# Kernel optimization log

Hardware: AMD Instinct MI355X
Metric: run time of the kernel (lower is better)

The kernel has to match this reference:

```python
import jax, jax.numpy as jnp
import numpy as np

B, L, D, K = 4, 512, 768, 96
H = 4 * D  # projection hidden width


def _proj(x, w1, b1, w2, b2):
    # create_projection_layer: Linear -> ReLU -> (Dropout, identity at eval) -> Linear
    return jnp.maximum(x @ w1 + b1, 0.0) @ w2 + b2


def setup_inputs() -> dict:
    key = jax.random.key(0)
    ks = jax.random.split(key, 12)
    g = lambda k, shape, fan: jax.random.normal(k, shape, jnp.float32) * (1.0 / np.sqrt(fan))
    inp = {
        "h": jax.random.normal(ks[0], (B, L, D), jnp.float32),
        "span_idx": jax.random.randint(ks[1], (B, K, 2), 0, L),
        "ps_w1": g(ks[2], (D, H), D), "ps_b1": jnp.zeros((H,), jnp.float32),
        "ps_w2": g(ks[3], (H, D), H), "ps_b2": jnp.zeros((D,), jnp.float32),
        "pe_w1": g(ks[4], (D, H), D), "pe_b1": jnp.zeros((H,), jnp.float32),
        "pe_w2": g(ks[5], (H, D), H), "pe_b2": jnp.zeros((D,), jnp.float32),
        "so_w1": g(ks[6], (2 * D, H), 2 * D), "so_b1": jnp.zeros((H,), jnp.float32),
        "so_w2": g(ks[7], (H, D), H), "so_b2": jnp.zeros((D,), jnp.float32),
        "ro_w1": g(ks[8], (2 * D, H), 2 * D), "ro_b1": jnp.zeros((H,), jnp.float32),
        "ro_w2": g(ks[9], (H, D), H), "ro_b2": jnp.zeros((D,), jnp.float32),
    }
    return inp


def _gather_tokens(rep, idx):
    # rep: [B,L,D], idx: [B,K] -> [B,K,D]
    b, k = idx.shape
    d = rep.shape[-1]
    return jnp.take_along_axis(rep, jnp.broadcast_to(idx[:, :, None], (b, k, d)), axis=1)


def reference(h, span_idx, ps_w1, ps_b1, ps_w2, ps_b2, pe_w1, pe_b1, pe_w2, pe_b2,
              so_w1, so_b1, so_w2, so_b2, ro_w1, ro_b1, ro_w2, ro_b2):
    # SpanMarkerV1
    start_rep = _proj(h, ps_w1, ps_b1, ps_w2, ps_b2)   # [B,L,D]
    end_rep = _proj(h, pe_w1, pe_b1, pe_w2, pe_b2)     # [B,L,D]
    st = _gather_tokens(start_rep, span_idx[:, :, 0])  # [B,K,D]
    en = _gather_tokens(end_rep, span_idx[:, :, 1])    # [B,K,D]
    cat = jnp.maximum(jnp.concatenate([st, en], axis=-1), 0.0)  # relu
    entity_reps = _proj(cat, so_w1, so_b1, so_w2, so_b2)        # [B,K,D]

    # off-diagonal pair enumeration, row-major (i,j) with i != j — static indices
    n = entity_reps.shape[1]
    idx = np.arange(n)
    ii = np.repeat(idx, n)
    jj = np.tile(idx, n)
    keep = ii != jj
    ii, jj = ii[keep], jj[keep]  # each length n*(n-1)
    pairs = jnp.concatenate([entity_reps[:, ii], entity_reps[:, jj]], axis=-1)  # [B,P,2D]
    return _proj(pairs, ro_w1, ro_b1, ro_w2, ro_b2)  # [B,P,D]
```

## Files before the change

### kernel.cpp

```cpp
#include <hip/hip_runtime.h>
#include <hip/hip_bf16.h>

#define Bdim 4
#define Ldim 512
#define Ddim 768
#define Kspan 96
#define Hdim 3072
#define Pdim 9120
#define MROWS 384
#define NKT 96

typedef __bf16 bf16x8 __attribute__((ext_vector_type(8)));
typedef float f32x4 __attribute__((ext_vector_type(4)));
typedef float f32x16 __attribute__((ext_vector_type(16)));
typedef unsigned short ushort8v __attribute__((ext_vector_type(8)));
typedef unsigned short ushort4v __attribute__((ext_vector_type(4)));

static __device__ __forceinline__ unsigned short f2bf(float x){
  return __builtin_bit_cast(unsigned short, (__bf16)x);
}
static __device__ __forceinline__ float bf2f(unsigned short u){
  return (float)__builtin_bit_cast(__bf16, u);
}

__global__ __launch_bounds__(256) void transpose_split(
    const float* __restrict__ W, unsigned short* __restrict__ WTh,
    unsigned short* __restrict__ WTl, int K, int N)
{
  __shared__ float tile[64][65];
  int k0 = blockIdx.y * 64, n0 = blockIdx.x * 64;
  int c = threadIdx.x & 63, r0 = threadIdx.x >> 6;
  for (int p = 0; p < 16; p++){
    int r = r0 + p * 4;
    tile[c][r] = W[(size_t)(k0 + r) * N + n0 + c];
  }
  __syncthreads();
  for (int p = 0; p < 16; p++){
    int n = r0 + p * 4;
    float x = tile[n][c];
    unsigned short h = f2bf(x);
    size_t o = (size_t)(n0 + n) * K + k0 + c;
    WTh[o] = h;
    WTl[o] = f2bf(x - bf2f(h));
  }
}

__global__ __launch_bounds__(256) void pack_w2(
    const float* __restrict__ W, unsigned short* __restrict__ W2P)
{
  __shared__ float tile[32][97];
  int kt = blockIdx.x, nq = blockIdx.y, t = threadIdx.x;
  for (int q = 0; q < 12; q++){
    int flat = q * 256 + t;
    int kl = flat / 96, n = flat - kl * 96;
    tile[kl][n] = W[(size_t)(kt * 32 + kl) * Ddim + nq * 96 + n];
  }
  __syncthreads();
  unsigned short* outp = W2P + ((size_t)(nq * 96 + kt)) * 3072;
  for (int q = 0; q < 12; q++){
    int o = q * 256 + t;
    int n = o >> 5, klx = o & 31;
    int kl = klx ^ ((n & 8) << 1);
    outp[o] = f2bf(tile[kl][n]);
  }
}

__global__ __launch_bounds__(256) void pack_v(
    const float* __restrict__ Vbuf, unsigned short* __restrict__ Vp)
{
  int kt = blockIdx.x, b = blockIdx.y, t = threadIdx.x;
  unsigned short* outp = Vp + ((size_t)(b * 96 + kt)) * 3072;
  for (int q = 0; q < 12; q++){
    int flat = q * 256 + t;
    int j = flat >> 5, kl = flat & 31;
    outp[flat] = f2bf(Vbuf[(size_t)(b * 96 + j) * Hdim + kt * 32 + kl]);
  }
}

__global__ __launch_bounds__(256) void gather_rows(
    const float* __restrict__ h, const int* __restrict__ span, float* __restrict__ hg)
{
  int x = blockIdx.x;
  int sel = (x >= MROWS) ? 1 : 0;
  int r = x - sel * MROWS;
  int b = r / Kspan, k = r - b * Kspan;
  int idx = span[(b * Kspan + k) * 2 + sel];
  const float* src = h + ((size_t)b * Ldim + idx) * Ddim;
  float* dst = hg + (size_t)x * Ddim;
  for (int d = threadIdx.x; d < Ddim; d += 256) dst[d] = src[d];
}

struct GJob {
  const float* A;
  const unsigned short* Wh;
  const unsigned short* Wl;
  const float* bias;
  float* C;
};

template<int MODE, int SPLIT>
__global__ __launch_bounds__(256) void gemm_ms(
    GJob j0, GJob j1, int ldA, int ldW, int ldC, int kLen, size_t csz)
{
  constexpr int SR = 40;
  __shared__ __align__(16) unsigned short Ah[64 * SR], Al[64 * SR];
  __shared__ __align__(16) unsigned short Bh[128 * SR], Bl[128 * SR];
  int zj, s;
  if (SPLIT == 1){ zj = blockIdx.z; s = 0; }
  else { zj = blockIdx.z / SPLIT; s = blockIdx.z % SPLIT; }
  const GJob J = zj ? j1 : j0;
  int kBegin = s * kLen;
  float* Cptr = (MODE == 2) ? (J.C + (size_t)s * csz) : J.C;

  int m0 = blockIdx.y * 64, n0 = blockIdx.x * 128;
  int t = threadIdx.x, lane = t & 63, wid = t >> 6;
  int wm = wid >> 1, wn = wid & 1;
  int lr = lane & 15, lk = (lane >> 4) * 8;
  f32x4 acc[2][4] = {};
  int ar = t >> 2, akq = t & 3;
  for (int k0 = 0; k0 < kLen; k0 += 32){
    {
      const float* sp = J.A + (size_t)(m0 + ar) * ldA + kBegin + k0 + akq * 8;
      f32x4 x0 = *(const f32x4*)sp, x1 = *(const f32x4*)(sp + 4);
      ushort8v vh, vl;
      for (int e = 0; e < 4; e++){ float x = x0[e]; unsigned short hh = f2bf(x); vh[e] = hh; vl[e] = f2bf(x - bf2f(hh)); }
      for (int e = 0; e < 4; e++){ float x = x1[e]; unsigned short hh = f2bf(x); vh[e+4] = hh; vl[e+4] = f2bf(x - bf2f(hh)); }
      *(ushort8v*)&Ah[ar * SR + akq * 8] = vh;
      *(ushort8v*)&Al[ar * SR + akq * 8] = vl;
    }
    for (int p = 0; p < 2; p++){
      int idx = p * 256 + t; int n = idx >> 2, kq = idx & 3;
      size_t go = (size_t)(n0 + n) * ldW + kBegin + k0 + kq * 8;
      *(ushort8v*)&Bh[n * SR + kq * 8] = *(const ushort8v*)(J.Wh + go);
      *(ushort8v*)&Bl[n * SR + kq * 8] = *(const ushort8v*)(J.Wl + go);
    }
    __syncthreads();
    bf16x8 ah[2], al2[2], bh[4], bl[4];
    for (int f = 0; f < 2; f++){ int o = (wm * 32 + f * 16 + lr) * SR + lk; ah[f] = *(const bf16x8*)&Ah[o]; al2[f] = *(const bf16x8*)&Al[o]; }
    for (int g = 0; g < 4; g++){ int o = (wn * 64 + g * 16 + lr) * SR + lk; bh[g] = *(const bf16x8*)&Bh[o]; bl[g] = *(const bf16x8*)&Bl[o]; }
    for (int f = 0; f < 2; f++)
      for (int g = 0; g < 4; g++){
        acc[f][g] = __builtin_amdgcn_mfma_f32_16x16x32_bf16(ah[f],  bh[g], acc[f][g], 0, 0, 0);
        acc[f][g] = __builtin_amdgcn_mfma_f32_16x16x32_bf16(ah[f],  bl[g], acc[f][g], 0, 0, 0);
        acc[f][g] = __builtin_amdgcn_mfma_f32_16x16x32_bf16(al2[f], bh[g], acc[f][g], 0, 0, 0);
      }
    __syncthreads();
  }
  int rr = (lane >> 4) * 4;
  for (int f = 0; f < 2; f++){
    int gm = m0 + wm * 32 + f * 16 + rr;
    for (int g = 0; g < 4; g++){
      int gn = n0 + wn * 64 + g * 16 + (lane & 15);
      float bv = (MODE != 2 && J.bias) ? J.bias[gn] : 0.f;
      for (int r2 = 0; r2 < 4; r2++){
        float v = acc[f][g][r2] + bv;
        if (MODE == 0) v = fmaxf(v, 0.f);
        Cptr[(size_t)(gm + r2) * ldC + gn] = v;
      }
    }
  }
}

template<bool RELU>
__global__ __launch_bounds__(256) void reduce_part(
    const float* __restrict__ P, int S,
    const float* __restrict__ bias0, const float* __restrict__ bias1,
    float* __restrict__ outp, int zCount, int ldOut)
{
  const int MN = MROWS * Ddim;
  int idx4 = blockIdx.x * 256 + threadIdx.x;
  int flat = idx4 * 4;
  if (flat >= MN * zCount) return;
  int z = flat / MN; int rem = flat - z * MN;
  int r = rem / Ddim; int c = rem - r * Ddim;
  const float* base = P + (size_t)z * S * MN + rem;
  f32x4 sv = *(const f32x4*)base;
  for (int ss = 1; ss < S; ss++){ f32x4 v = *(const f32x4*)(base + (size_t)ss * MN); sv += v; }
  const float* bp = z ? bias1 : bias0;
  f32x4 bv = *(const f32x4*)(bp + c);
  sv += bv;
  if (RELU) for (int e = 0; e < 4; e++) sv[e] = fmaxf(sv[e], 0.f);
  *(f32x4*)(outp + (size_t)r * ldOut + z * Ddim + c) = sv;
}

__global__ __launch_bounds__(256, 2) void pair_gemm3(
    const float* __restrict__ U,
    const unsigned short* __restrict__ Vp,
    const unsigned short* __restrict__ W2P,
    const float* __restrict__ b2,
    float* __restrict__ out)
{
  __shared__ __align__(16) unsigned short As[2][384 * 32];
  __shared__ __align__(16) unsigned short Bs[2][96 * 32];

  int x = blockIdx.x;
  int nq = x & 7;
  int l = x >> 3;
  int b = l / 24;
  int iq = l - b * 24;

  int t = threadIdx.x, lane = t & 63, w = t >> 6;
  int kq = t & 7, jb = t >> 3;

  ushort4v vld[3];
  f32x4 uld[4];
  f32x16 acc[3][3] = {};

  auto issueB = [&](int kt, int buf){
    const unsigned short* tb = W2P + ((size_t)(nq * 96 + kt)) * 3072;
    #pragma unroll
    for (int s2 = 0; s2 < 2; s2++){
      int seg = w + s2 * 4;
      if (seg < 6){
        const unsigned short* src = tb + seg * 512 + lane * 8;
        unsigned int* dst = (unsigned int*)&Bs[buf][seg * 512 + lane * 8];
        __builtin_amdgcn_global_load_lds(
            (const __attribute__((address_space(1))) unsigned int*)src,
            (__attribute__((address_space(3))) unsigned int*)dst, 16, 0, 0);
      }
    }
  };
  auto issueUV = [&](int kt){
    const unsigned short* vb = Vp + ((size_t)(b * 96 + kt)) * 3072 + kq * 4;
    #pragma unroll
    for (int q = 0; q < 3; q++)
      vld[q] = *(const ushort4v*)(vb + (q * 32 + jb) * 32);
    const float* ub = U + ((size_t)(b * 96 + iq * 4)) * Hdim + kt * 32 + kq * 4;
    #pragma unroll
    for (int g = 0; g < 4; g++)
      uld[g] = *(const f32x4*)(ub + (size_t)g * Hdim);
  };
  auto buildA = [&](int buf){
    #pragma unroll
    for (int q = 0; q < 3; q++){
      int j = q * 32 + jb;
      f32x4 vf;
      #pragma unroll
      for (int e = 0; e < 4; e++) vf[e] = bf2f(vld[q][e]);
      #pragma unroll
      for (int g = 0; g < 4; g++){
        int row = g * 96 + j;
        ushort4v pk;
        #pragma unroll
        for (int e = 0; e < 4; e++) pk[e] = f2bf(fmaxf(uld[g][e] + vf[e], 0.f));
        int idx = row * 32 + ((kq * 4) ^ ((row & 8) << 1));
        *(ushort4v*)&As[buf][idx] = pk;
      }
    }
  };
  auto mfmaPhase = [&](int buf){
    #pragma unroll
    for (int kh = 0; kh < 2; kh++){
      int gg = kh * 2 + (lane >> 5);
      bf16x8 af[3], bfr[3];
      #pragma unroll
      for (int mf = 0; mf < 3; mf++){
        int row = w * 96 + mf * 32 + (lane & 31);
        af[mf] = *(const bf16x8*)&As[buf][row * 32 + ((gg * 8) ^ ((row & 8) << 1))];
      }
      #pragma unroll
      for (int nf = 0; nf < 3; nf++){
        int n = nf * 32 + (lane & 31);
        bfr[nf] = *(const bf16x8*)&Bs[buf][n * 32 + ((gg * 8) ^ ((n & 8) << 1))];
      }
      __builtin_amdgcn_s_setprio(1);
      #pragma unroll
      for (int mf = 0; mf < 3; mf++)
        #pragma unroll
        for (int nf = 0; nf < 3; nf++)
          acc[mf][nf] = __builtin_amdgcn_mfma_f32_32x32x16_bf16(af[mf], bfr[nf], acc[mf][nf], 0, 0, 0);
      __builtin_amdgcn_s_setprio(0);
    }
  };

  issueB(0, 0);
  issueUV(0);
  buildA(0);
  __syncthreads();

  for (int kt = 0; kt < NKT; kt++){
    int cur = kt & 1;
    if (kt + 1 < NKT){ issueB(kt + 1, cur ^ 1); issueUV(kt + 1); }
    mfmaPhase(cur);
    if (kt + 1 < NKT) buildA(cur ^ 1);
    __syncthreads();
  }

  int i = iq * 4 + w;
  size_t outB = (size_t)b * Pdim;
  int colbase = nq * 96;
  float bc[3];
  #pragma unroll
  for (int nf = 0; nf < 3; nf++) bc[nf] = b2[colbase + nf * 32 + (lane & 31)];
  #pragma unroll
  for (int mf = 0; mf < 3; mf++){
    #pragma unroll
    for (int reg = 0; reg < 16; reg++){
      int j = mf * 32 + (reg & 3) + 8 * (reg >> 2) + 4 * (lane >> 5);
      if (j == i) continue;
      int p = i * 95 + j - (j > i ? 1 : 0);
      float* orow = out + (outB + p) * Ddim + colbase;
      #pragma unroll
      for (int nf = 0; nf < 3; nf++){
        int cn = nf * 32 + (lane & 31);
        orow[cn] = acc[mf][nf][reg] + bc[nf];
      }
    }
  }
}

extern "C" void kernel_launch(void* const* d_in, const int* in_sizes, int n_in,
                              void* d_out, int out_size, void* d_ws, size_t ws_size,
                              hipStream_t stream)
{
  (void)in_sizes; (void)n_in; (void)out_size;
  const float* h     = (const float*)d_in[0];
  const int*   span  = (const int*)d_in[1];
  const float* ps_w1 = (const float*)d_in[2];
  const float* ps_b1 = (const float*)d_in[3];
  const float* ps_w2 = (const float*)d_in[4];
  const float* ps_b2 = (const float*)d_in[5];
  const float* pe_w1 = (const float*)d_in[6];
  const float* pe_b1 = (const float*)d_in[7];
  const float* pe_w2 = (const float*)d_in[8];
  const float* pe_b2 = (const float*)d_in[9];
  const float* so_w1 = (const float*)d_in[10];
  const float* so_b1 = (const float*)d_in[11];
  const float* so_w2 = (const float*)d_in[12];
  const float* so_b2 = (const float*)d_in[13];
  const float* ro_w1 = (const float*)d_in[14];
  const float* ro_b1 = (const float*)d_in[15];
  const float* ro_w2 = (const float*)d_in[16];
  const float* ro_b2 = (const float*)d_in[17];

  char* ws = (char*)d_ws;
  size_t off = 0;
  auto alloc_us = [&](size_t n)->unsigned short*{
    unsigned short* p = (unsigned short*)(ws + off);
    off += ((n * 2 + 255) & ~(size_t)255);
    return p;
  };
  auto alloc_f = [&](size_t n)->float*{
    float* p = (float*)(ws + off);
    off += ((n * 4 + 255) & ~(size_t)255);
    return p;
  };

  unsigned short* ps1h = alloc_us((size_t)Hdim * Ddim); unsigned short* ps1l = alloc_us((size_t)Hdim * Ddim);
  unsigned short* ps2h = alloc_us((size_t)Ddim * Hdim); unsigned short* ps2l = alloc_us((size_t)Ddim * Hdim);
  unsigned short* pe1h = alloc_us((size_t)Hdim * Ddim); unsigned short* pe1l = alloc_us((size_t)Hdim * Ddim);
  unsigned short* pe2h = alloc_us((size_t)Ddim * Hdim); unsigned short* pe2l = alloc_us((size_t)Ddim * Hdim);
  unsigned short* so1h = alloc_us((size_t)Hdim * 2 * Ddim); unsigned short* so1l = alloc_us((size_t)Hdim * 2 * Ddim);
  unsigned short* so2h = alloc_us((size_t)Ddim * Hdim); unsigned short* so2l = alloc_us((size_t)Ddim * Hdim);
  unsigned short* ro1h = alloc_us((size_t)Hdim * 2 * Ddim); unsigned short* ro1l = alloc_us((size_t)Hdim * 2 * Ddim);
  unsigned short* W2P  = alloc_us((size_t)Ddim * Hdim);
  unsigned short* Vp   = alloc_us((size_t)Bdim * Kspan * Hdim);
  float* hg     = alloc_f((size_t)2 * MROWS * Ddim);
  float* mid_s  = alloc_f((size_t)MROWS * Hdim);
  float* mid_e  = alloc_f((size_t)MROWS * Hdim);
  float* cat    = alloc_f((size_t)MROWS * 2 * Ddim);
  float* entity = alloc_f((size_t)MROWS * Ddim);
  float* Ubuf   = alloc_f((size_t)MROWS * Hdim);
  float* Vbuf   = alloc_f((size_t)MROWS * Hdim);
  const size_t MN = (size_t)MROWS * Ddim;
  float* P2 = alloc_f(8 * MN);
  float* P3 = alloc_f(4 * MN);
  if (off > ws_size) return;

  dim3 tb(256);
  transpose_split<<<dim3(Hdim/64, Ddim/64), tb, 0, stream>>>(ps_w1, ps1h, ps1l, Ddim, Hdim);
  transpose_split<<<dim3(Ddim/64, Hdim/64), tb, 0, stream>>>(ps_w2, ps2h, ps2l, Hdim, Ddim);
  transpose_split<<<dim3(Hdim/64, Ddim/64), tb, 0, stream>>>(pe_w1, pe1h, pe1l, Ddim, Hdim);
  transpose_split<<<dim3(Ddim/64, Hdim/64), tb, 0, stream>>>(pe_w2, pe2h, pe2l, Hdim, Ddim);
  transpose_split<<<dim3(Hdim/64, (2*Ddim)/64), tb, 0, stream>>>(so_w1, so1h, so1l, 2*Ddim, Hdim);
  transpose_split<<<dim3(Ddim/64, Hdim/64), tb, 0, stream>>>(so_w2, so2h, so2l, Hdim, Ddim);
  transpose_split<<<dim3(Hdim/64, (2*Ddim)/64), tb, 0, stream>>>(ro_w1, ro1h, ro1l, 2*Ddim, Hdim);
  pack_w2<<<dim3(NKT, 8), tb, 0, stream>>>(ro_w2, W2P);

  gather_rows<<<2 * MROWS, tb, 0, stream>>>(h, span, hg);

  {
    GJob j0{hg,                      ps1h, ps1l, ps_b1, mid_s};
    GJob j1{hg + (size_t)MROWS*Ddim, pe1h, pe1l, pe_b1, mid_e};
    gemm_ms<0,1><<<dim3(Hdim/128, MROWS/64, 2), tb, 0, stream>>>(j0, j1, Ddim, Ddim, Hdim, Ddim, 0);
  }
  {
    GJob j0{mid_s, ps2h, ps2l, nullptr, P2};
    GJob j1{mid_e, pe2h, pe2l, nullptr, P2 + 4*MN};
    gemm_ms<2,4><<<dim3(Ddim/128, MROWS/64, 8), tb, 0, stream>>>(j0, j1, Hdim, Hdim, Ddim, Hdim/4, MN);
  }
  reduce_part<true><<<(2*(int)MN)/1024, tb, 0, stream>>>(P2, 4, ps_b2, pe_b2, cat, 2, 2*Ddim);
  {
    GJob j0{cat, so1h, so1l, so_b1, mid_s};
    gemm_ms<0,1><<<dim3(Hdim/128, MROWS/64, 1), tb, 0, stream>>>(j0, j0, 2*Ddim, 2*Ddim, Hdim, 2*Ddim, 0);
  }
  {
    GJob j0{mid_s, so2h, so2l, nullptr, P3};
    gemm_ms<2,4><<<dim3(Ddim/128, MROWS/64, 4), tb, 0, stream>>>(j0, j0, Hdim, Hdim, Ddim, Hdim/4, MN);
  }
  reduce_part<false><<<((int)MN)/1024, tb, 0, stream>>>(P3, 4, so_b2, so_b2, entity, 1, Ddim);
  {
    GJob j0{entity, ro1h,        ro1l,        ro_b1,   Ubuf};
    GJob j1{entity, ro1h + Ddim, ro1l + Ddim, nullptr, Vbuf};
    gemm_ms<1,1><<<dim3(Hdim/128, MROWS/64, 2), tb, 0, stream>>>(j0, j1, Ddim, 2*Ddim, Hdim, Ddim, 0);
  }
  pack_v<<<dim3(NKT, Bdim), tb, 0, stream>>>(Vbuf, Vp);

  pair_gemm3<<<768, tb, 0, stream>>>(Ubuf, Vp, W2P, ro_b2, (float*)d_out);
}
```

Before: 531.1 us.

## Build pair activations in registers from LDS-staged V, widen K-tile to 64

The pair GEMM no longer materialises the relu(U+V) A-tile in shared memory. Each wave now loads its U row into registers, streams bf16 V and W2 tiles into LDS asynchronously, and forms the A fragments directly before the MFMA. The K tile grows from 32 to 64 and the tile shape moves to 2 pair-rows × 192 output columns. The packing layouts and XOR swizzles change to match, and the seven weight transposes are merged into one multi-job launch. The aim is to remove the LDS write/read round-trip and per-tile sync overhead of building A, at the cost of redundant per-wave conversion work and a different block-to-data mapping.

Measured after the change: 470.7 us. 11.4% less time.

```diff
diff --git a/kernel.cpp b/kernel.cpp
--- a/kernel.cpp
+++ b/kernel.cpp
@@ -8,13 +8,12 @@
 #define Hdim 3072
 #define Pdim 9120
 #define MROWS 384
-#define NKT 96
+#define NKT4 48
 
 typedef __bf16 bf16x8 __attribute__((ext_vector_type(8)));
 typedef float f32x4 __attribute__((ext_vector_type(4)));
 typedef float f32x16 __attribute__((ext_vector_type(16)));
 typedef unsigned short ushort8v __attribute__((ext_vector_type(8)));
-typedef unsigned short ushort4v __attribute__((ext_vector_type(4)));
 
 static __device__ __forceinline__ unsigned short f2bf(float x){
   return __builtin_bit_cast(unsigned short, (__bf16)x);
@@ -22,46 +21,58 @@
 static __device__ __forceinline__ float bf2f(unsigned short u){
   return (float)__builtin_bit_cast(__bf16, u);
 }
-
-__global__ __launch_bounds__(256) void transpose_split(
-    const float* __restrict__ W, unsigned short* __restrict__ WTh,
-    unsigned short* __restrict__ WTl, int K, int N)
-{
+static __device__ __forceinline__ float bfbits2f(unsigned short u){
+  return __builtin_bit_cast(float, (unsigned)u << 16);
+}
+
+struct TJob { const float* W; unsigned short* Th; unsigned short* Tl; int K; int N; int base; };
+struct TJobs { TJob j[7]; };
+
+__global__ __launch_bounds__(256) void transpose_multi(TJobs JJ)
+{
+  int x = blockIdx.x;
+  int ji = 0;
+  #pragma unroll
+  for (int q = 1; q < 7; q++) if (x >= JJ.j[q].base) ji = q;
+  TJob J = JJ.j[ji];
+  int local = x - J.base;
+  int tilesX = J.N >> 6;
+  int bx = local % tilesX, by = local / tilesX;
   __shared__ float tile[64][65];
-  int k0 = blockIdx.y * 64, n0 = blockIdx.x * 64;
+  int k0 = by * 64, n0 = bx * 64;
   int c = threadIdx.x & 63, r0 = threadIdx.x >> 6;
   for (int p = 0; p < 16; p++){
     int r = r0 + p * 4;
-    tile[c][r] = W[(size_t)(k0 + r) * N + n0 + c];
+    tile[c][r] = J.W[(size_t)(k0 + r) * J.N + n0 + c];
   }
   __syncthreads();
   for (int p = 0; p < 16; p++){
     int n = r0 + p * 4;
-    float x = tile[n][c];
-    unsigned short h = f2bf(x);
-    size_t o = (size_t)(n0 + n) * K + k0 + c;
-    WTh[o] = h;
-    WTl[o] = f2bf(x - bf2f(h));
+    float xv = tile[n][c];
+    unsigned short h = f2bf(xv);
+    size_t o = (size_t)(n0 + n) * J.K + k0 + c;
+    J.Th[o] = h;
+    J.Tl[o] = f2bf(xv - bf2f(h));
   }
 }
 
 __global__ __launch_bounds__(256) void pack_w2(
     const float* __restrict__ W, unsigned short* __restrict__ W2P)
 {
-  __shared__ float tile[32][97];
+  __shared__ float tile[64][193];
   int kt = blockIdx.x, nq = blockIdx.y, t = threadIdx.x;
-  for (int q = 0; q < 12; q++){
+  for (int q = 0; q < 48; q++){
     int flat = q * 256 + t;
-    int kl = flat / 96, n = flat - kl * 96;
-    tile[kl][n] = W[(size_t)(kt * 32 + kl) * Ddim + nq * 96 + n];
+    int ks = flat / 192, n = flat - ks * 192;
+    tile[ks][n] = W[(size_t)(kt * 64 + ks) * Ddim + nq * 192 + n];
   }
   __syncthreads();
-  unsigned short* outp = W2P + ((size_t)(nq * 96 + kt)) * 3072;
-  for (int q = 0; q < 12; q++){
+  unsigned short* outp = W2P + (size_t)(nq * 48 + kt) * 12288;
+  for (int q = 0; q < 48; q++){
     int o = q * 256 + t;
-    int n = o >> 5, klx = o & 31;
-    int kl = klx ^ ((n & 8) << 1);
-    outp[o] = f2bf(tile[kl][n]);
+    int n = o >> 6, kph = o & 63;
+    int ks = kph ^ ((n & 7) << 3);
+    outp[o] = f2bf(tile[ks][n]);
   }
 }
 
@@ -69,11 +80,19 @@
     const float* __restrict__ Vbuf, unsigned short* __restrict__ Vp)
 {
   int kt = blockIdx.x, b = blockIdx.y, t = threadIdx.x;
-  unsigned short* outp = Vp + ((size_t)(b * 96 + kt)) * 3072;
-  for (int q = 0; q < 12; q++){
-    int flat = q * 256 + t;
-    int j = flat >> 5, kl = flat & 31;
-    outp[flat] = f2bf(Vbuf[(size_t)(b * 96 + j) * Hdim + kt * 32 + kl]);
+  unsigned short* outp = Vp + (size_t)(b * 48 + kt) * 6144;
+  #pragma unroll
+  for (int q = 0; q < 3; q++){
+    int item = q * 256 + t;
+    int j = item >> 3, g = item & 7;
+    const float* src = Vbuf + (size_t)(b * 96 + j) * Hdim + kt * 64 + g * 8;
+    f32x4 a0 = *(const f32x4*)src, a1 = *(const f32x4*)(src + 4);
+    ushort8v pk;
+    #pragma unroll
+    for (int e = 0; e < 4; e++) pk[e] = f2bf(a0[e]);
+    #pragma unroll
+    for (int e = 0; e < 4; e++) pk[e + 4] = f2bf(a1[e]);
+    *(ushort8v*)(outp + j * 64 + ((g ^ (j & 7)) << 3)) = pk;
   }
 }
 
@@ -183,128 +202,116 @@
   *(f32x4*)(outp + (size_t)r * ldOut + z * Ddim + c) = sv;
 }
 
-__global__ __launch_bounds__(256, 2) void pair_gemm3(
+__global__ __launch_bounds__(256, 2) void pair_gemm4(
     const float* __restrict__ U,
     const unsigned short* __restrict__ Vp,
     const unsigned short* __restrict__ W2P,
     const float* __restrict__ b2,
     float* __restrict__ out)
 {
-  __shared__ __align__(16) unsigned short As[2][384 * 32];
-  __shared__ __align__(16) unsigned short Bs[2][96 * 32];
+  __shared__ __align__(16) unsigned short Bs[2][12288];
+  __shared__ __align__(16) unsigned short Vs[2][6144];
 
   int x = blockIdx.x;
-  int nq = x & 7;
-  int l = x >> 3;
-  int b = l / 24;
-  int iq = l - b * 24;
+  int xcd = x & 7;
+  int s = x >> 3;
+  int combo = xcd + ((s >= 48) ? 8 : 0);
+  int ig = (s >= 48) ? (s - 48) : s;
+  int nq = combo & 3, b = combo >> 2;
 
   int t = threadIdx.x, lane = t & 63, w = t >> 6;
-  int kq = t & 7, jb = t >> 3;
-
-  ushort4v vld[3];
-  f32x4 uld[4];
+  int wm = w >> 1, wn = w & 1;
+  int l31 = lane & 31, hsel = lane >> 5;
+  int i = ig * 2 + wm;
+  const float* Urow = U + ((size_t)(b * 96 + i)) * Hdim + hsel * 8;
+
   f32x16 acc[3][3] = {};
 
   auto issueB = [&](int kt, int buf){
-    const unsigned short* tb = W2P + ((size_t)(nq * 96 + kt)) * 3072;
-    #pragma unroll
-    for (int s2 = 0; s2 < 2; s2++){
-      int seg = w + s2 * 4;
-      if (seg < 6){
-        const unsigned short* src = tb + seg * 512 + lane * 8;
-        unsigned int* dst = (unsigned int*)&Bs[buf][seg * 512 + lane * 8];
-        __builtin_amdgcn_global_load_lds(
-            (const __attribute__((address_space(1))) unsigned int*)src,
-            (__attribute__((address_space(3))) unsigned int*)dst, 16, 0, 0);
+    const unsigned short* srcb = W2P + (size_t)(nq * 48 + kt) * 12288 + t * 8;
+    #pragma unroll
+    for (int q = 0; q < 6; q++){
+      __builtin_amdgcn_global_load_lds(
+          (const __attribute__((address_space(1))) unsigned int*)(srcb + q * 2048),
+          (__attribute__((address_space(3))) unsigned int*)&Bs[buf][q * 2048 + t * 8],
+          16, 0, 0);
+    }
+  };
+  auto issueV = [&](int kt, int buf){
+    const unsigned short* srcv = Vp + (size_t)(b * 48 + kt) * 6144 + t * 8;
+    #pragma unroll
+    for (int q = 0; q < 3; q++){
+      __builtin_amdgcn_global_load_lds(
+          (const __attribute__((address_space(1))) unsigned int*)(srcv + q * 2048),
+          (__attribute__((address_space(3))) unsigned int*)&Vs[buf][q * 2048 + t * 8],
+          16, 0, 0);
+    }
+  };
+
+  issueB(0, 0);
+  issueV(0, 0);
+  __syncthreads();
+
+  for (int kt = 0; kt < NKT4; kt++){
+    int cur = kt & 1;
+    if (kt + 1 < NKT4){ issueB(kt + 1, cur ^ 1); issueV(kt + 1, cur ^ 1); }
+
+    float uf[4][8];
+    {
+      const float* ub = Urow + kt * 64;
+      #pragma unroll
+      for (int kh = 0; kh < 4; kh++){
+        *(f32x4*)&uf[kh][0] = *(const f32x4*)(ub + kh * 16);
+        *(f32x4*)&uf[kh][4] = *(const f32x4*)(ub + kh * 16 + 4);
       }
     }
-  };
-  auto issueUV = [&](int kt){
-    const unsigned short* vb = Vp + ((size_t)(b * 96 + kt)) * 3072 + kq * 4;
-    #pragma unroll
-    for (int q = 0; q < 3; q++)
-      vld[q] = *(const ushort4v*)(vb + (q * 32 + jb) * 32);
-    const float* ub = U + ((size_t)(b * 96 + iq * 4)) * Hdim + kt * 32 + kq * 4;
-    #pragma unroll
-    for (int g = 0; g < 4; g++)
-      uld[g] = *(const f32x4*)(ub + (size_t)g * Hdim);
-  };
-  auto buildA = [&](int buf){
-    #pragma unroll
-    for (int q = 0; q < 3; q++){
-      int j = q * 32 + jb;
-      f32x4 vf;
+
+    #pragma unroll
+    for (int kh = 0; kh < 4; kh++){
+      int gx16 = (kh * 2 + hsel) * 16;
+      bf16x8 bfr[3], afr[3];
       #pragma unroll
-      for (int e = 0; e < 4; e++) vf[e] = bf2f(vld[q][e]);
-      #pragma unroll
-      for (int g = 0; g < 4; g++){
-        int row = g * 96 + j;
-        ushort4v pk;
-        #pragma unroll
-        for (int e = 0; e < 4; e++) pk[e] = f2bf(fmaxf(uld[g][e] + vf[e], 0.f));
-        int idx = row * 32 + ((kq * 4) ^ ((row & 8) << 1));
-        *(ushort4v*)&As[buf][idx] = pk;
+      for (int nf = 0; nf < 3; nf++){
+        int n = wn * 96 + nf * 32 + l31;
+        bfr[nf] = *(const bf16x8*)((const char*)&Bs[cur][0] + n * 128 + (gx16 ^ ((n & 7) << 4)));
       }
-    }
-  };
-  auto mfmaPhase = [&](int buf){
-    #pragma unroll
-    for (int kh = 0; kh < 2; kh++){
-      int gg = kh * 2 + (lane >> 5);
-      bf16x8 af[3], bfr[3];
       #pragma unroll
       for (int mf = 0; mf < 3; mf++){
-        int row = w * 96 + mf * 32 + (lane & 31);
-        af[mf] = *(const bf16x8*)&As[buf][row * 32 + ((gg * 8) ^ ((row & 8) << 1))];
-      }
-      #pragma unroll
-      for (int nf = 0; nf < 3; nf++){
-        int n = nf * 32 + (lane & 31);
-        bfr[nf] = *(const bf16x8*)&Bs[buf][n * 32 + ((gg * 8) ^ ((n & 8) << 1))];
+        int j = mf * 32 + l31;
+        ushort8v vv = *(const ushort8v*)((const char*)&Vs[cur][0] + j * 128 + (gx16 ^ ((j & 7) << 4)));
+        ushort8v pk;
+        #pragma unroll
+        for (int e = 0; e < 8; e++)
+          pk[e] = f2bf(fmaxf(uf[kh][e] + bfbits2f(vv[e]), 0.f));
+        afr[mf] = __builtin_bit_cast(bf16x8, pk);
       }
       __builtin_amdgcn_s_setprio(1);
       #pragma unroll
       for (int mf = 0; mf < 3; mf++)
         #pragma unroll
         for (int nf = 0; nf < 3; nf++)
-          acc[mf][nf] = __builtin_amdgcn_mfma_f32_32x32x16_bf16(af[mf], bfr[nf], acc[mf][nf], 0, 0, 0);
+          acc[mf][nf] = __builtin_amdgcn_mfma_f32_32x32x16_bf16(afr[mf], bfr[nf], acc[mf][nf], 0, 0, 0);
       __builtin_amdgcn_s_setprio(0);
     }
-  };
-
-  issueB(0, 0);
-  issueUV(0);
-  buildA(0);
-  __syncthreads();
-
-  for (int kt = 0; kt < NKT; kt++){
-    int cur = kt & 1;
-    if (kt + 1 < NKT){ issueB(kt + 1, cur ^ 1); issueUV(kt + 1); }
-    mfmaPhase(cur);
-    if (kt + 1 < NKT) buildA(cur ^ 1);
     __syncthreads();
   }
 
-  int i = iq * 4 + w;
   size_t outB = (size_t)b * Pdim;
-  int colbase = nq * 96;
+  int colbase = nq * 192 + wn * 96;
   float bc[3];
   #pragma unroll
-  for (int nf = 0; nf < 3; nf++) bc[nf] = b2[colbase + nf * 32 + (lane & 31)];
+  for (int nf = 0; nf < 3; nf++) bc[nf] = b2[colbase + nf * 32 + l31];
   #pragma unroll
   for (int mf = 0; mf < 3; mf++){
     #pragma unroll
     for (int reg = 0; reg < 16; reg++){
-      int j = mf * 32 + (reg & 3) + 8 * (reg >> 2) + 4 * (lane >> 5);
+      int j = mf * 32 + (reg & 3) + 8 * (reg >> 2) + 4 * hsel;
       if (j == i) continue;
       int p = i * 95 + j - (j > i ? 1 : 0);
       float* orow = out + (outB + p) * Ddim + colbase;
       #pragma unroll
-      for (int nf = 0; nf < 3; nf++){
-        int cn = nf * 32 + (lane & 31);
-        orow[cn] = acc[mf][nf][reg] + bc[nf];
-      }
+      for (int nf = 0; nf < 3; nf++)
+        orow[nf * 32 + l31] = acc[mf][nf][reg] + bc[nf];
     }
   }
 }
@@ -353,8 +360,8 @@
   unsigned short* so1h = alloc_us((size_t)Hdim * 2 * Ddim); unsigned short* so1l = alloc_us((size_t)Hdim * 2 * Ddim);
   unsigned short* so2h = alloc_us((size_t)Ddim * Hdim); unsigned short* so2l = alloc_us((size_t)Ddim * Hdim);
   unsigned short* ro1h = alloc_us((size_t)Hdim * 2 * Ddim); unsigned short* ro1l = alloc_us((size_t)Hdim * 2 * Ddim);
-  unsigned short* W2P  = alloc_us((size_t)Ddim * Hdim);
-  unsigned short* Vp   = alloc_us((size_t)Bdim * Kspan * Hdim);
+  unsigned short* W2P  = alloc_us((size_t)4 * 48 * 12288);
+  unsigned short* Vp   = alloc_us((size_t)4 * 48 * 6144);
   float* hg     = alloc_f((size_t)2 * MROWS * Ddim);
   float* mid_s  = alloc_f((size_t)MROWS * Hdim);
   float* mid_e  = alloc_f((size_t)MROWS * Hdim);
@@ -368,14 +375,24 @@
   if (off > ws_size) return;
 
   dim3 tb(256);
-  transpose_split<<<dim3(Hdim/64, Ddim/64), tb, 0, stream>>>(ps_w1, ps1h, ps1l, Ddim, Hdim);
-  transpose_split<<<dim3(Ddim/64, Hdim/64), tb, 0, stream>>>(ps_w2, ps2h, ps2l, Hdim, Ddim);
-  transpose_split<<<dim3(Hdim/64, Ddim/64), tb, 0, stream>>>(pe_w1, pe1h, pe1l, Ddim, Hdim);
-  transpose_split<<<dim3(Ddim/64, Hdim/64), tb, 0, stream>>>(pe_w2, pe2h, pe2l, Hdim, Ddim);
-  transpose_split<<<dim3(Hdim/64, (2*Ddim)/64), tb, 0, stream>>>(so_w1, so1h, so1l, 2*Ddim, Hdim);
-  transpose_split<<<dim3(Ddim/64, Hdim/64), tb, 0, stream>>>(so_w2, so2h, so2l, Hdim, Ddim);
-  transpose_split<<<dim3(Hdim/64, (2*Ddim)/64), tb, 0, stream>>>(ro_w1, ro1h, ro1l, 2*Ddim, Hdim);
-  pack_w2<<<dim3(NKT, 8), tb, 0, stream>>>(ro_w2, W2P);
+
+  {
+    TJobs JJ;
+    int base = 0;
+    auto add = [&](int idx, const float* W, unsigned short* Th, unsigned short* Tl, int K, int N){
+      JJ.j[idx] = TJob{W, Th, Tl, K, N, base};
+      base += (N / 64) * (K / 64);
+    };
+    add(0, ps_w1, ps1h, ps1l, Ddim, Hdim);
+    add(1, ps_w2, ps2h, ps2l, Hdim, Ddim);
+    add(2, pe_w1, pe1h, pe1l, Ddim, Hdim);
+    add(3, pe_w2, pe2h, pe2l, Hdim, Ddim);
+    add(4, so_w1, so1h, so1l, 2 * Ddim, Hdim);
+    add(5, so_w2, so2h, so2l, Hdim, Ddim);
+    add(6, ro_w1, ro1h, ro1l, 2 * Ddim, Hdim);
+    transpose_multi<<<base, tb, 0, stream>>>(JJ);
+  }
+  pack_w2<<<dim3(NKT4, 4), tb, 0, stream>>>(ro_w2, W2P);
 
   gather_rows<<<2 * MROWS, tb, 0, stream>>>(h, span, hg);
 
@@ -404,7 +421,7 @@
     GJob j1{entity, ro1h + Ddim, ro1l + Ddim, nullptr, Vbuf};
     gemm_ms<1,1><<<dim3(Hdim/128, MROWS/64, 2), tb, 0, stream>>>(j0, j1, Ddim, 2*Ddim, Hdim, Ddim, 0);
   }
-  pack_v<<<dim3(NKT, Bdim), tb, 0, stream>>>(Vbuf, Vp);
-
-  pair_gemm3<<<768, tb, 0, stream>>>(Ubuf, Vp, W2P, ro_b2, (float*)d_out);
-}
+  pack_v<<<dim3(NKT4, Bdim), tb, 0, stream>>>(Vbuf, Vp);
+
+  pair_gemm4<<<768, tb, 0, stream>>>(Ubuf, Vp, W2P, ro_b2, (float*)d_out);
+}
```
